# Performance work log

Hardware: AMD Instinct MI355X
Metric: run time of the kernel (lower is better)

Reference implementation:

```python
import jax, jax.numpy as jnp
import numpy as np

N_NODES = 50000
N_EDGES = 800000
D = 128

def setup_inputs() -> dict:
    key = jax.random.key(0)
    k1, k2, k3, k4 = jax.random.split(key, 4)
    x = jax.random.normal(k1, (N_NODES, D), dtype=jnp.float32)
    edge_index = jax.random.randint(k2, (2, N_EDGES), 0, N_NODES, dtype=jnp.int64)
    # nn.Linear params: W is (out_dim, in_dim), b is (out_dim,)
    W = jax.random.normal(k3, (D, D), dtype=jnp.float32) * (1.0 / np.sqrt(D))
    b = jax.random.normal(k4, (D,), dtype=jnp.float32) * 0.01
    return {"x": x, "edge_index": edge_index, "W": W, "b": b}

def reference(x, edge_index, W, b):
    row, col = edge_index[0], edge_index[1]
    h = x @ W.T + b                      # (N, D) linear projection
    msgs = h[col]                        # gather by source col, (E, D)
    agg = jax.ops.segment_sum(msgs, row, num_segments=N_NODES)  # scatter-add by row
    return agg + h                       # residual
```

## Files before the change

### kernel.cpp

```cpp
#include <hip/hip_runtime.h>

#define NN 50000
#define NE 800000
#define DD 128

#define NBUCK 782
#define CAPB 1280
#define NBA 64
#define TPB_BIN 1024
#define EITER 13
#define ASTRIDE 132

typedef __attribute__((ext_vector_type(8))) short short8;
typedef __attribute__((ext_vector_type(4))) float f32x4;

__device__ __forceinline__ unsigned short f2bf(float f) {
    unsigned int u = __float_as_uint(f);
    u += 0x7fffu + ((u >> 16) & 1u);
    return (unsigned short)(u >> 16);
}

#define ACCUM8(a, pq)                                   \
    a[0] += __uint_as_float((pq).x << 16);              \
    a[1] += __uint_as_float((pq).x & 0xffff0000u);      \
    a[2] += __uint_as_float((pq).y << 16);              \
    a[3] += __uint_as_float((pq).y & 0xffff0000u);      \
    a[4] += __uint_as_float((pq).z << 16);              \
    a[5] += __uint_as_float((pq).z & 0xffff0000u);      \
    a[6] += __uint_as_float((pq).w << 16);              \
    a[7] += __uint_as_float((pq).w & 0xffff0000u);

__global__ __launch_bounds__(256) void prologue(
    const float* __restrict__ x, unsigned short* __restrict__ xbf,
    const float* __restrict__ W, unsigned short* __restrict__ Wbf,
    int* __restrict__ cursor)
{
    const int t = blockIdx.x * 256 + threadIdx.x;
    for (int i = t; i < NN * DD / 4; i += 512 * 256) {
        const float4 v = ((const float4*)x)[i];
        ushort4 s;
        s.x = f2bf(v.x); s.y = f2bf(v.y); s.z = f2bf(v.z); s.w = f2bf(v.w);
        ((ushort4*)xbf)[i] = s;
    }
    if (blockIdx.x == 0) {
        for (int i = threadIdx.x; i < DD * DD / 4; i += 256) {
            const float4 v = ((const float4*)W)[i];
            ushort4 s;
            s.x = f2bf(v.x); s.y = f2bf(v.y); s.z = f2bf(v.z); s.w = f2bf(v.w);
            ((ushort4*)Wbf)[i] = s;
        }
        for (int i = threadIdx.x; i < NBUCK; i += 256) cursor[i] = i * CAPB;
    }
}

__global__ __launch_bounds__(1024) void binpass(
    const int* __restrict__ ei, unsigned int* __restrict__ binned,
    int* __restrict__ cursor)
{
    __shared__ int cnt[NBUCK];
    __shared__ int off[NBUCK];
    const int t = threadIdx.x;
    if (t < NBUCK) cnt[t] = 0;
    __syncthreads();

    int rr[EITER], cc[EITER];
#pragma unroll
    for (int q = 0; q < EITER; ++q) {
        const int e = blockIdx.x * TPB_BIN + t + q * (NBA * TPB_BIN);
        rr[q] = (e < NE) ? ei[e] : -1;
        cc[q] = (e < NE) ? ei[NE + e] : 0;
    }
#pragma unroll
    for (int q = 0; q < EITER; ++q)
        if (rr[q] >= 0) atomicAdd(&cnt[rr[q] >> 6], 1);
    __syncthreads();

    if (t < NBUCK) off[t] = atomicAdd(&cursor[t], cnt[t]);
    __syncthreads();

#pragma unroll
    for (int q = 0; q < EITER; ++q) {
        if (rr[q] >= 0) {
            const int bk = rr[q] >> 6;
            const int p = atomicAdd(&off[bk], 1);
            if (p < (bk + 1) * CAPB && p < NBUCK * CAPB)
                binned[p] = ((unsigned)(rr[q] & 63) << 16) | (unsigned)cc[q];
        }
    }
}

__global__ __launch_bounds__(512) void aggemm(
    const unsigned short* __restrict__ xbf,
    const unsigned short* __restrict__ Wbf, const float* __restrict__ bias,
    const int* __restrict__ cursor, const unsigned int* __restrict__ binned,
    float* __restrict__ out)
{
    __shared__ float acc_l[64 * ASTRIDE];
    __shared__ unsigned int elist[CAPB];
    __shared__ int cnt_l[64];
    __shared__ int start_l[64];
    __shared__ int off_l[64];

    const int b     = blockIdx.x;
    const int node0 = b << 6;
    const int t     = threadIdx.x;
    const int wave  = t >> 6;
    const int lane  = t & 63;

    if (t < 64) cnt_l[t] = 0;
    __syncthreads();

    int cntb = cursor[b] - b * CAPB;
    if (cntb > CAPB) cntb = CAPB;
    const unsigned int* bptr = binned + (size_t)b * CAPB;

    unsigned int ue[3];
#pragma unroll
    for (int q = 0; q < 3; ++q) {
        const int e = q * 512 + t;
        ue[q] = 0u;
        if (e < cntb) {
            ue[q] = bptr[e];
            atomicAdd(&cnt_l[(ue[q] >> 16) & 63], 1);
        }
    }
    __syncthreads();

    if (t < 64) {
        const int orig = cnt_l[t];
        int v = orig;
#pragma unroll
        for (int d = 1; d < 64; d <<= 1) {
            const int o = __shfl_up(v, d, 64);
            if (t >= d) v += o;
        }
        start_l[t] = v - orig;
        off_l[t]   = v - orig;
    }
    __syncthreads();

#pragma unroll
    for (int q = 0; q < 3; ++q) {
        const int e = q * 512 + t;
        if (e < cntb) {
            const int p = atomicAdd(&off_l[(ue[q] >> 16) & 63], 1);
            elist[p] = ue[q];
        }
    }
    __syncthreads();

    const int g = lane >> 4;
    const int s = lane & 15;

#pragma unroll
    for (int r2 = 0; r2 < 8; ++r2) {
        const int ln = wave * 8 + r2;
        const int st = start_l[ln];
        const int dn = cnt_l[ln];

        float a[8];
#pragma unroll
        for (int i = 0; i < 8; ++i) a[i] = 0.f;

        uint4 p[8];
#pragma unroll
        for (int q = 0; q < 8; ++q) {
            const int e = q * 4 + g;
            p[q] = (uint4){0u, 0u, 0u, 0u};
            if (e < dn) {
                const unsigned u = elist[st + e];
                p[q] = *(const uint4*)(xbf + (size_t)(u & 0xffffu) * 128 + s * 8);
            }
        }
#pragma unroll
        for (int q = 0; q < 8; ++q) { ACCUM8(a, p[q]); }

        for (int k = 32; k < dn; k += 16) {
            uint4 pp[4];
#pragma unroll
            for (int q = 0; q < 4; ++q) {
                const int e = k + q * 4 + g;
                pp[q] = (uint4){0u, 0u, 0u, 0u};
                if (e < dn) {
                    const unsigned u = elist[st + e];
                    pp[q] = *(const uint4*)(xbf + (size_t)(u & 0xffffu) * 128 + s * 8);
                }
            }
#pragma unroll
            for (int q = 0; q < 4; ++q) { ACCUM8(a, pp[q]); }
        }

#pragma unroll
        for (int i = 0; i < 8; ++i) a[i] += __shfl_xor(a[i], 16, 64);
#pragma unroll
        for (int i = 0; i < 8; ++i) a[i] += __shfl_xor(a[i], 32, 64);

        if (g == 0) {
            const int grow = node0 + ln;
            if (grow < NN) {
                const uint4 sv = *(const uint4*)(xbf + (size_t)grow * 128 + s * 8);
                ACCUM8(a, sv);
            }
            *(float4*)&acc_l[ln * ASTRIDE + s * 8]     = (float4){a[0], a[1], a[2], a[3]};
            *(float4*)&acc_l[ln * ASTRIDE + s * 8 + 4] = (float4){a[4], a[5], a[6], a[7]};
            if (s == 0) acc_l[ln * ASTRIDE + 128] = (float)(dn + 1);
        }
    }
    __syncthreads();

    const int m16  = lane & 15;
    const int quad = lane >> 4;
    const int rowt = (wave & 3) * 16;
    const int colb = (wave >> 2) * 64;

    short8 af[4];
#pragma unroll
    for (int kc = 0; kc < 4; ++kc) {
        const float* src = &acc_l[(rowt + m16) * ASTRIDE + kc * 32 + quad * 8];
        const float4 a0 = *(const float4*)src;
        const float4 a1 = *(const float4*)(src + 4);
        short8 a;
        a[0] = (short)f2bf(a0.x); a[1] = (short)f2bf(a0.y);
        a[2] = (short)f2bf(a0.z); a[3] = (short)f2bf(a0.w);
        a[4] = (short)f2bf(a1.x); a[5] = (short)f2bf(a1.y);
        a[6] = (short)f2bf(a1.z); a[7] = (short)f2bf(a1.w);
        af[kc] = a;
    }

    f32x4 ac[4];
#pragma unroll
    for (int nt = 0; nt < 4; ++nt) ac[nt] = (f32x4){0.f, 0.f, 0.f, 0.f};

#pragma unroll
    for (int kc = 0; kc < 4; ++kc) {
#pragma unroll
        for (int nt = 0; nt < 4; ++nt) {
            const short8 bf = *(const short8*)(
                Wbf + (size_t)(colb + nt * 16 + m16) * 128 + kc * 32 + quad * 8);
            ac[nt] = __builtin_amdgcn_mfma_f32_16x16x32_bf16(af[kc], bf, ac[nt], 0, 0, 0);
        }
    }

    float bv[4];
#pragma unroll
    for (int nt = 0; nt < 4; ++nt) bv[nt] = bias[colb + nt * 16 + m16];

#pragma unroll
    for (int r = 0; r < 4; ++r) {
        const int lr   = rowt + quad * 4 + r;
        const int grow = node0 + lr;
        if (grow < NN) {
            const float cd = acc_l[lr * ASTRIDE + 128];
#pragma unroll
            for (int nt = 0; nt < 4; ++nt)
                out[(size_t)grow * 128 + colb + nt * 16 + m16] = ac[nt][r] + cd * bv[nt];
        }
    }
}

extern "C" void kernel_launch(void* const* d_in, const int* in_sizes, int n_in,
                              void* d_out, int out_size, void* d_ws, size_t ws_size,
                              hipStream_t stream)
{
    const float* x  = (const float*)d_in[0];
    const int*   ei = (const int*)d_in[1];
    const float* W  = (const float*)d_in[2];
    const float* b  = (const float*)d_in[3];
    float* out = (float*)d_out;

    unsigned short* xbf    = (unsigned short*)d_ws;
    unsigned int*   binned = (unsigned int*)(xbf + (size_t)NN * DD);
    unsigned short* Wbf    = (unsigned short*)(binned + (size_t)NBUCK * CAPB);
    int*            cursor = (int*)(Wbf + DD * DD);

    prologue<<<512, 256, 0, stream>>>(x, xbf, W, Wbf, cursor);

    binpass<<<NBA, TPB_BIN, 0, stream>>>(ei, binned, cursor);

    aggemm<<<NBUCK, 512, 0, stream>>>(xbf, Wbf, b, cursor, binned, out);
}
```

Measured before the change: 147.8 us.

## Fuse bf16 conversion and edge binning into one kernel, memset cursors

Merges the x/W bf16 conversion kernel and the edge-binning kernel into a single launch. The first 64 blocks bin edges and the remaining 192 blocks convert x and W, so the two independent jobs run concurrently instead of back to back. Cursor initialisation moves to a hipMemsetAsync, with cursors now storing per-bucket counts rather than absolute offsets. The aggregation kernel also issues the self-row load early and skips gathers and accumulations for unused unrolled slots. The risk is a memset launch replacing a kernel, and reduced bandwidth for the conversion now that it has fewer blocks.

```diff
diff --git a/kernel.cpp b/kernel.cpp
--- a/kernel.cpp
+++ b/kernel.cpp
@@ -7,7 +7,8 @@
 #define NBUCK 782
 #define CAPB 1280
 #define NBA 64
-#define TPB_BIN 1024
+#define NBC 192
+#define TPB_PREP 1024
 #define EITER 13
 #define ASTRIDE 132
 
@@ -30,61 +31,61 @@
     a[6] += __uint_as_float((pq).w << 16);              \
     a[7] += __uint_as_float((pq).w & 0xffff0000u);
 
-__global__ __launch_bounds__(256) void prologue(
+__global__ __launch_bounds__(1024) void prep(
     const float* __restrict__ x, unsigned short* __restrict__ xbf,
     const float* __restrict__ W, unsigned short* __restrict__ Wbf,
-    int* __restrict__ cursor)
-{
-    const int t = blockIdx.x * 256 + threadIdx.x;
-    for (int i = t; i < NN * DD / 4; i += 512 * 256) {
-        const float4 v = ((const float4*)x)[i];
-        ushort4 s;
-        s.x = f2bf(v.x); s.y = f2bf(v.y); s.z = f2bf(v.z); s.w = f2bf(v.w);
-        ((ushort4*)xbf)[i] = s;
-    }
-    if (blockIdx.x == 0) {
-        for (int i = threadIdx.x; i < DD * DD / 4; i += 256) {
-            const float4 v = ((const float4*)W)[i];
-            ushort4 s;
-            s.x = f2bf(v.x); s.y = f2bf(v.y); s.z = f2bf(v.z); s.w = f2bf(v.w);
-            ((ushort4*)Wbf)[i] = s;
-        }
-        for (int i = threadIdx.x; i < NBUCK; i += 256) cursor[i] = i * CAPB;
-    }
-}
-
-__global__ __launch_bounds__(1024) void binpass(
     const int* __restrict__ ei, unsigned int* __restrict__ binned,
     int* __restrict__ cursor)
 {
     __shared__ int cnt[NBUCK];
     __shared__ int off[NBUCK];
     const int t = threadIdx.x;
-    if (t < NBUCK) cnt[t] = 0;
-    __syncthreads();
-
-    int rr[EITER], cc[EITER];
-#pragma unroll
-    for (int q = 0; q < EITER; ++q) {
-        const int e = blockIdx.x * TPB_BIN + t + q * (NBA * TPB_BIN);
-        rr[q] = (e < NE) ? ei[e] : -1;
-        cc[q] = (e < NE) ? ei[NE + e] : 0;
-    }
-#pragma unroll
-    for (int q = 0; q < EITER; ++q)
-        if (rr[q] >= 0) atomicAdd(&cnt[rr[q] >> 6], 1);
-    __syncthreads();
-
-    if (t < NBUCK) off[t] = atomicAdd(&cursor[t], cnt[t]);
-    __syncthreads();
-
-#pragma unroll
-    for (int q = 0; q < EITER; ++q) {
-        if (rr[q] >= 0) {
-            const int bk = rr[q] >> 6;
-            const int p = atomicAdd(&off[bk], 1);
-            if (p < (bk + 1) * CAPB && p < NBUCK * CAPB)
-                binned[p] = ((unsigned)(rr[q] & 63) << 16) | (unsigned)cc[q];
+
+    if (blockIdx.x < NBA) {
+        if (t < NBUCK) cnt[t] = 0;
+        __syncthreads();
+
+        int rr[EITER], cc[EITER];
+#pragma unroll
+        for (int q = 0; q < EITER; ++q) {
+            const int e = blockIdx.x * TPB_PREP + t + q * (NBA * TPB_PREP);
+            rr[q] = (e < NE) ? ei[e] : -1;
+            cc[q] = (e < NE) ? ei[NE + e] : 0;
+        }
+#pragma unroll
+        for (int q = 0; q < EITER; ++q)
+            if (rr[q] >= 0) atomicAdd(&cnt[rr[q] >> 6], 1);
+        __syncthreads();
+
+        if (t < NBUCK) off[t] = atomicAdd(&cursor[t], cnt[t]);
+        __syncthreads();
+
+#pragma unroll
+        for (int q = 0; q < EITER; ++q) {
+            if (rr[q] >= 0) {
+                const int bk = rr[q] >> 6;
+                const int p = atomicAdd(&off[bk], 1);
+                if (p < CAPB)
+                    binned[(size_t)bk * CAPB + p] =
+                        ((unsigned)(rr[q] & 63) << 16) | (unsigned)cc[q];
+            }
+        }
+        return;
+    }
+
+    const int ct = (blockIdx.x - NBA) * TPB_PREP + t;
+    for (int i = ct; i < NN * DD / 4; i += NBC * TPB_PREP) {
+        const float4 v = ((const float4*)x)[i];
+        ushort4 s;
+        s.x = f2bf(v.x); s.y = f2bf(v.y); s.z = f2bf(v.z); s.w = f2bf(v.w);
+        ((ushort4*)xbf)[i] = s;
+    }
+    if (blockIdx.x == NBA) {
+        for (int i = t; i < DD * DD / 4; i += TPB_PREP) {
+            const float4 v = ((const float4*)W)[i];
+            ushort4 s;
+            s.x = f2bf(v.x); s.y = f2bf(v.y); s.z = f2bf(v.z); s.w = f2bf(v.w);
+            ((ushort4*)Wbf)[i] = s;
         }
     }
 }
@@ -110,7 +111,7 @@
     if (t < 64) cnt_l[t] = 0;
     __syncthreads();
 
-    int cntb = cursor[b] - b * CAPB;
+    int cntb = cursor[b];
     if (cntb > CAPB) cntb = CAPB;
     const unsigned int* bptr = binned + (size_t)b * CAPB;
 
@@ -157,23 +158,31 @@
         const int ln = wave * 8 + r2;
         const int st = start_l[ln];
         const int dn = cnt_l[ln];
+        const int grow = node0 + ln;
+
+        uint4 sv = (uint4){0u, 0u, 0u, 0u};
+        if (g == 0 && grow < NN)
+            sv = *(const uint4*)(xbf + (size_t)grow * 128 + s * 8);
 
         float a[8];
 #pragma unroll
         for (int i = 0; i < 8; ++i) a[i] = 0.f;
+
+        const int nq = (dn + 3) >> 2;
 
         uint4 p[8];
 #pragma unroll
         for (int q = 0; q < 8; ++q) {
             const int e = q * 4 + g;
             p[q] = (uint4){0u, 0u, 0u, 0u};
-            if (e < dn) {
+            if (q < nq && e < dn) {
                 const unsigned u = elist[st + e];
                 p[q] = *(const uint4*)(xbf + (size_t)(u & 0xffffu) * 128 + s * 8);
             }
         }
 #pragma unroll
-        for (int q = 0; q < 8; ++q) { ACCUM8(a, p[q]); }
+        for (int q = 0; q < 8; ++q)
+            if (q < nq) { ACCUM8(a, p[q]); }
 
         for (int k = 32; k < dn; k += 16) {
             uint4 pp[4];
@@ -196,11 +205,7 @@
         for (int i = 0; i < 8; ++i) a[i] += __shfl_xor(a[i], 32, 64);
 
         if (g == 0) {
-            const int grow = node0 + ln;
-            if (grow < NN) {
-                const uint4 sv = *(const uint4*)(xbf + (size_t)grow * 128 + s * 8);
-                ACCUM8(a, sv);
-            }
+            ACCUM8(a, sv);
             *(float4*)&acc_l[ln * ASTRIDE + s * 8]     = (float4){a[0], a[1], a[2], a[3]};
             *(float4*)&acc_l[ln * ASTRIDE + s * 8 + 4] = (float4){a[4], a[5], a[6], a[7]};
             if (s == 0) acc_l[ln * ASTRIDE + 128] = (float)(dn + 1);
@@ -273,9 +278,9 @@
     unsigned short* Wbf    = (unsigned short*)(binned + (size_t)NBUCK * CAPB);
     int*            cursor = (int*)(Wbf + DD * DD);
 
-    prologue<<<512, 256, 0, stream>>>(x, xbf, W, Wbf, cursor);
-
-    binpass<<<NBA, TPB_BIN, 0, stream>>>(ei, binned, cursor);
+    hipMemsetAsync(cursor, 0, NBUCK * sizeof(int), stream);
+
+    prep<<<NBA + NBC, TPB_PREP, 0, stream>>>(x, xbf, W, Wbf, ei, binned, cursor);
 
     aggemm<<<NBUCK, 512, 0, stream>>>(xbf, Wbf, b, cursor, binned, out);
 }
```

After: 140.2 us. 5.1% less time.
